# Kernel optimization log

Hardware: AMD Instinct MI355X
Metric: run time of the kernel (lower is better)

## Reference

```python
import jax, jax.numpy as jnp
import numpy as np

D_MODEL = 1024
N_HEADS = 16


def setup_inputs() -> dict:
    key = jax.random.key(0)
    ks = jax.random.split(key, 11)
    B, L, D = 2, 2048, D_MODEL
    s = 1.0 / np.sqrt(D)
    return {
        "q": jax.random.normal(ks[0], (B, L, D), jnp.float32),
        "k": jax.random.normal(ks[1], (B, L, D), jnp.float32),
        "v": jax.random.normal(ks[2], (B, L, D), jnp.float32),
        "w_q": jax.random.normal(ks[3], (D, D), jnp.float32) * s,
        "b_q": jnp.zeros((D,), jnp.float32),
        "w_k": jax.random.normal(ks[4], (D, D), jnp.float32) * s,
        "b_k": jnp.zeros((D,), jnp.float32),
        "w_v": jax.random.normal(ks[5], (D, D), jnp.float32) * s,
        "b_v": jnp.zeros((D,), jnp.float32),
        "w_o": jax.random.normal(ks[6], (D, D), jnp.float32) * s,
        "b_o": jnp.zeros((D,), jnp.float32),
    }


def reference(q, k, v, w_q, b_q, w_k, b_k, w_v, b_v, w_o, b_o):
    B, L, D = q.shape
    H = N_HEADS
    d_h = D // H
    # QKV projections (nn.Linear: x @ W^T + b)
    qh = (q @ w_q.T + b_q).reshape(B, L, H, d_h).transpose(0, 2, 1, 3)  # [B,H,L,d_h]
    kh = (k @ w_k.T + b_k).reshape(B, L, H, d_h).transpose(0, 2, 1, 3)
    vh = (v @ w_v.T + b_v).reshape(B, L, H, d_h).transpose(0, 2, 1, 3)
    # scaled dot-product attention
    scores = jnp.einsum('bhqd,bhkd->bhqk', qh, kh) / jnp.sqrt(jnp.float32(d_h))
    attn = jax.nn.softmax(scores, axis=-1)                               # [B,H,L,L]
    ctx = jnp.einsum('bhqk,bhkd->bhqd', attn, vh)                        # [B,H,L,d_h]
    ctx = ctx.transpose(0, 2, 1, 3).reshape(B, L, D)
    out = ctx @ w_o.T + b_o
    return out, attn
```

## Files before the change

### kernel.cpp

```cpp
#include <hip/hip_runtime.h>
#include <hip/hip_bf16.h>
#include <stdint.h>

#define DEV static __device__ __forceinline__

typedef float f32x4 __attribute__((ext_vector_type(4)));
typedef __bf16 bf16x8 __attribute__((ext_vector_type(8)));
typedef unsigned short u16x8 __attribute__((ext_vector_type(8)));
typedef unsigned short u16x4 __attribute__((ext_vector_type(4)));
typedef uint32_t u32x2 __attribute__((ext_vector_type(2)));
typedef uint32_t u32x4 __attribute__((ext_vector_type(4)));
typedef unsigned short u16;

#define B_ 2
#define L_ 2048
#define D_MODEL_ 1024
#define H_ 16
#define DH_ 64

#define SHIFT2 11.5415603f

DEV u16 f2bf(float f) {
  union { float f; uint32_t u; } v; v.f = f;
  uint32_t r = v.u + 0x7FFFu + ((v.u >> 16) & 1u);
  return (u16)(r >> 16);
}

DEV float exp2v(float x) {
#if __has_builtin(__builtin_amdgcn_exp2f)
  return __builtin_amdgcn_exp2f(x);
#else
  float r;
  asm("v_exp_f32 %0, %1" : "=v"(r) : "v"(x));
  return r;
#endif
}

DEV uint32_t pkbf(float a, float b) {
  __hip_bfloat162 h = __float22bfloat162_rn(float2{a, b});
  union { __hip_bfloat162 h; uint32_t u; } cv; cv.h = h;
  return cv.u;
}

DEV f32x4 mfma16(bf16x8 a, bf16x8 b, f32x4 c) {
  return __builtin_amdgcn_mfma_f32_16x16x32_bf16(a, b, c, 0, 0, 0);
}

DEV void gl_lds16(const void* g, void* l) {
  __builtin_amdgcn_global_load_lds(
      (const __attribute__((address_space(1))) unsigned int*)g,
      (__attribute__((address_space(3))) unsigned int*)l, 16, 0, 0);
}

struct CastArgs {
  const float* src[7];
  u16* dst[7];
  int n8[7];
};

__global__ __launch_bounds__(256) void cast_kernel(CastArgs a) {
  const int z = blockIdx.z;
  const float* s = a.src[z];
  u16* d = a.dst[z];
  const int n8 = a.n8[z];
  const int stride = gridDim.x * blockDim.x;
  for (int i = blockIdx.x * blockDim.x + threadIdx.x; i < n8; i += stride) {
    const float4* sp = (const float4*)s + (size_t)i * 2;
    float4 x0 = sp[0], x1 = sp[1];
    u16x8 o;
    o[0] = f2bf(x0.x); o[1] = f2bf(x0.y); o[2] = f2bf(x0.z); o[3] = f2bf(x0.w);
    o[4] = f2bf(x1.x); o[5] = f2bf(x1.y); o[6] = f2bf(x1.z); o[7] = f2bf(x1.w);
    *((u16x8*)d + i) = o;
  }
}

#define GM 4096
#define GN 1024
#define GK 1024

struct GemmArgs {
  const u16* X[3];
  const u16* W[3];
  const float* bias[3];
  void* out[3];
  float alpha[3];
  int mode[3];
};

__global__ __launch_bounds__(256) void gemm_bt(GemmArgs g) {
  const int z = blockIdx.z;
  const u16* X = g.X[z];
  const u16* W = g.W[z];
  const float* bias = g.bias[z];
  const float alpha = g.alpha[z];
  const int mode = g.mode[z];
  const int m0 = blockIdx.y * 128, n0 = blockIdx.x * 128;

  __shared__ __align__(16) char smem[32 * 1024];
  char* As = smem;
  char* Bs = smem + 16 * 1024;

  const int tid = threadIdx.x;
  const int lane = tid & 63, w = tid >> 6;
  const int l15 = lane & 15, l4 = lane >> 4;
  const int wm = (w >> 1) * 64, wn = (w & 1) * 64;

  f32x4 acc[4][4];
#pragma unroll
  for (int i = 0; i < 4; ++i)
#pragma unroll
    for (int j = 0; j < 4; ++j) acc[i][j] = f32x4{0.f, 0.f, 0.f, 0.f};

  for (int ks = 0; ks < GK; ks += 64) {
    __syncthreads();
    for (int c = w; c < 16; c += 4) {
      int r = c * 8 + (lane >> 3);
      int j = lane & 7;
      int sj = j ^ (r & 7);
      gl_lds16((const char*)(X + (size_t)(m0 + r) * GK + ks) + sj * 16, As + c * 1024);
      gl_lds16((const char*)(W + (size_t)(n0 + r) * GK + ks) + sj * 16, Bs + c * 1024);
    }
    __syncthreads();
#pragma unroll
    for (int ksub = 0; ksub < 2; ++ksub) {
      bf16x8 af[4], bfr[4];
#pragma unroll
      for (int mf = 0; mf < 4; ++mf) {
        int r = wm + mf * 16 + l15;
        int j16 = ksub * 4 + l4;
        af[mf] = *(const bf16x8*)(As + r * 128 + ((j16 ^ (r & 7)) * 16));
      }
#pragma unroll
      for (int nf = 0; nf < 4; ++nf) {
        int r = wn + nf * 16 + l15;
        int j16 = ksub * 4 + l4;
        bfr[nf] = *(const bf16x8*)(Bs + r * 128 + ((j16 ^ (r & 7)) * 16));
      }
#pragma unroll
      for (int mf = 0; mf < 4; ++mf)
#pragma unroll
        for (int nf = 0; nf < 4; ++nf) acc[mf][nf] = mfma16(af[mf], bfr[nf], acc[mf][nf]);
    }
  }

  if (mode == 2) {
    u16* base = (u16*)g.out[z];
#pragma unroll
    for (int nf = 0; nf < 4; ++nf) {
      int n = n0 + wn + nf * 16 + l15;
      float bv = bias[n];
#pragma unroll
      for (int mf = 0; mf < 4; ++mf) {
        int m = m0 + wm + mf * 16 + l4 * 4;
        u16x4 pk;
#pragma unroll
        for (int r = 0; r < 4; ++r) pk[r] = f2bf((acc[mf][nf][r] + bv) * alpha);
        size_t off = (((size_t)(m >> 11) * H_ + (n >> 6)) * DH_ + (n & 63)) * (size_t)L_ + (m & 2047);
        *(u16x4*)(base + off) = pk;
      }
    }
  } else {
#pragma unroll
    for (int nf = 0; nf < 4; ++nf) {
      int n = n0 + wn + nf * 16 + l15;
      float bv = bias[n];
#pragma unroll
      for (int mf = 0; mf < 4; ++mf) {
#pragma unroll
        for (int r = 0; r < 4; ++r) {
          int m = m0 + wm + mf * 16 + l4 * 4 + r;
          float val = (acc[mf][nf][r] + bv) * alpha;
          if (mode == 1)
            ((float*)g.out[z])[(size_t)m * GN + n] = val;
          else
            ((u16*)g.out[z])[(size_t)m * GN + n] = f2bf(val);
        }
      }
    }
  }
}

__global__ __launch_bounds__(256) void attn_kernel(const u16* Qp, const u16* Kp,
                                                   const u16* VT, float* attn,
                                                   u16* ctx) {
  const int q0 = blockIdx.x * 64;
  const int h = blockIdx.y, b = blockIdx.z;
  const int tid = threadIdx.x, lane = tid & 63, w = tid >> 6;
  const int l15 = lane & 15, l4 = lane >> 4;
  const int lr = lane >> 3, lj = lane & 7;

  __shared__ __align__(16) char smem[32 * 1024];
  char* Pw = smem + w * 4096;

  const u16* Qbase = Qp + ((size_t)(b * L_ + q0 + w * 16) * D_MODEL_ + h * DH_);
  const u16* Kbase = Kp + ((size_t)(b * L_) * D_MODEL_ + h * DH_);
  const u16* Vb = VT + ((size_t)((b * H_ + h) * DH_) * L_);
  float* attnb = attn + ((size_t)(b * H_ + h)) * L_ * L_;

  auto stK = [&](int t) {
    const int c0 = t * 64, bsel = (t & 1) << 13;
    for (int c = w; c < 8; c += 4) {
      int r = c * 8 + lr, sj = lj ^ (r & 7);
      gl_lds16((const char*)(Kbase + (size_t)(c0 + r) * D_MODEL_) + sj * 16,
               smem + 16384 + bsel + c * 1024);
    }
  };

  bf16x8 qa[2];
#pragma unroll
  for (int ksub = 0; ksub < 2; ++ksub)
    qa[ksub] = *(const bf16x8*)(Qbase + (size_t)l15 * D_MODEL_ + (ksub * 4 + l4) * 8);

  stK(0);
  __syncthreads();

  float ssum = 0.f;
  for (int t = 0; t < 32; ++t) {
    if (t < 31) stK(t + 1);
    const char* Ks = smem + 16384 + ((t & 1) << 13);
    f32x4 s[4];
#pragma unroll
    for (int nf = 0; nf < 4; ++nf) s[nf] = f32x4{0.f, 0.f, 0.f, 0.f};
    __builtin_amdgcn_s_setprio(1);
#pragma unroll
    for (int ksub = 0; ksub < 2; ++ksub) {
      int j16 = ksub * 4 + l4;
      bf16x8 kb[4];
#pragma unroll
      for (int nf = 0; nf < 4; ++nf) {
        int r = nf * 16 + l15;
        kb[nf] = *(const bf16x8*)(Ks + r * 128 + ((j16 ^ (r & 7)) * 16));
      }
#pragma unroll
      for (int nf = 0; nf < 4; ++nf) s[nf] = mfma16(kb[nf], qa[ksub], s[nf]);
    }
    __builtin_amdgcn_s_setprio(0);
#pragma unroll
    for (int nf = 0; nf < 4; ++nf)
#pragma unroll
      for (int r = 0; r < 4; ++r) ssum += exp2v(s[nf][r] - SHIFT2);
    __syncthreads();
  }

  stK(0);

  ssum += __shfl_xor(ssum, 16);
  ssum += __shfl_xor(ssum, 32);
  const float c2 = SHIFT2 + __log2f(ssum);

  f32x4 cacc[4];
#pragma unroll
  for (int i = 0; i < 4; ++i) cacc[i] = f32x4{0.f, 0.f, 0.f, 0.f};
  __syncthreads();

  const int swz = l15 & 7;
  float* awave = attnb + (size_t)(q0 + w * 16) * L_;

  for (int t = 0; t < 32; ++t) {
    const int c0 = t * 64;
    if (t < 31) stK(t + 1);
    bf16x8 va[2][4];
#pragma unroll
    for (int ksub = 0; ksub < 2; ++ksub)
#pragma unroll
      for (int df = 0; df < 4; ++df)
        va[ksub][df] = *(const bf16x8*)(Vb + (size_t)(df * 16 + l15) * L_ + c0 +
                                        (ksub * 4 + l4) * 8);
    __builtin_amdgcn_sched_barrier(0);

    const char* Ks = smem + 16384 + ((t & 1) << 13);
    f32x4 s[4];
#pragma unroll
    for (int nf = 0; nf < 4; ++nf) s[nf] = f32x4{0.f, 0.f, 0.f, 0.f};
    __builtin_amdgcn_s_setprio(1);
#pragma unroll
    for (int ksub = 0; ksub < 2; ++ksub) {
      int j16 = ksub * 4 + l4;
      bf16x8 kb[4];
#pragma unroll
      for (int nf = 0; nf < 4; ++nf) {
        int r = nf * 16 + l15;
        kb[nf] = *(const bf16x8*)(Ks + r * 128 + ((j16 ^ (r & 7)) * 16));
      }
#pragma unroll
      for (int nf = 0; nf < 4; ++nf) s[nf] = mfma16(kb[nf], qa[ksub], s[nf]);
    }
    __builtin_amdgcn_s_setprio(0);

#pragma unroll
    for (int nf = 0; nf < 4; ++nf) {
      f32x4 p4;
#pragma unroll
      for (int r = 0; r < 4; ++r) p4[r] = exp2v(s[nf][r] - c2);
      *(f32x4*)(Pw + l15 * 256 + (((nf * 4 + l4) ^ swz) * 16)) = p4;
    }
#pragma unroll
    for (int j = 0; j < 4; ++j) {
      int row = 4 * j + (lane >> 4);
      f32x4 v = *(const f32x4*)(Pw + row * 256 + (((lane & 15) ^ (row & 7)) * 16));
      __builtin_nontemporal_store(
          v, (f32x4*)(awave + (size_t)row * L_ + c0 + (lane & 15) * 4));
    }
    __builtin_amdgcn_s_setprio(1);
#pragma unroll
    for (int ksub = 0; ksub < 2; ++ksub) {
      int cbase = (ksub * 4 + l4) * 2;
      f32x4 plo = *(const f32x4*)(Pw + l15 * 256 + ((cbase ^ swz) * 16));
      f32x4 phi = *(const f32x4*)(Pw + l15 * 256 + (((cbase + 1) ^ swz) * 16));
      union { u32x4 u; bf16x8 h; } pa;
      pa.u[0] = pkbf(plo[0], plo[1]);
      pa.u[1] = pkbf(plo[2], plo[3]);
      pa.u[2] = pkbf(phi[0], phi[1]);
      pa.u[3] = pkbf(phi[2], phi[3]);
#pragma unroll
      for (int df = 0; df < 4; ++df)
        cacc[df] = mfma16(pa.h, va[ksub][df], cacc[df]);
    }
    __builtin_amdgcn_s_setprio(0);
    if (t < 31) {
      asm volatile("s_waitcnt vmcnt(12)" ::: "memory");
      __builtin_amdgcn_s_barrier();
      __builtin_amdgcn_sched_barrier(0);
    }
  }

#pragma unroll
  for (int df = 0; df < 4; ++df) {
#pragma unroll
    for (int r = 0; r < 4; ++r) {
      int row = q0 + w * 16 + l4 * 4 + r;
      int col = h * DH_ + df * 16 + l15;
      ctx[(size_t)(b * L_ + row) * D_MODEL_ + col] = f2bf(cacc[df][r]);
    }
  }
}

extern "C" void kernel_launch(void* const* d_in, const int* in_sizes, int n_in,
                              void* d_out, int out_size, void* d_ws, size_t ws_size,
                              hipStream_t stream) {
  const float* q = (const float*)d_in[0];
  const float* k = (const float*)d_in[1];
  const float* v = (const float*)d_in[2];
  const float* w_q = (const float*)d_in[3];
  const float* b_q = (const float*)d_in[4];
  const float* w_k = (const float*)d_in[5];
  const float* b_k = (const float*)d_in[6];
  const float* w_v = (const float*)d_in[7];
  const float* b_v = (const float*)d_in[8];
  const float* w_o = (const float*)d_in[9];
  const float* b_o = (const float*)d_in[10];

  float* out = (float*)d_out;
  float* attn = (float*)d_out + (size_t)B_ * L_ * D_MODEL_;

  const size_t MB = 1u << 20;
  char* ws = (char*)d_ws;
  u16* qb = (u16*)(ws + 0 * MB);
  u16* kb = (u16*)(ws + 8 * MB);
  u16* vb = (u16*)(ws + 16 * MB);
  u16* wqb = (u16*)(ws + 24 * MB);
  u16* wkb = (u16*)(ws + 26 * MB);
  u16* wvb = (u16*)(ws + 28 * MB);
  u16* wob = (u16*)(ws + 30 * MB);
  u16* Qp = (u16*)(ws + 32 * MB);
  u16* Kp = (u16*)(ws + 40 * MB);
  u16* VT = (u16*)(ws + 48 * MB);
  u16* ctx = kb;

  CastArgs ca;
  ca.src[0] = q;   ca.dst[0] = qb;  ca.n8[0] = (B_ * L_ * D_MODEL_) / 8;
  ca.src[1] = k;   ca.dst[1] = kb;  ca.n8[1] = (B_ * L_ * D_MODEL_) / 8;
  ca.src[2] = v;   ca.dst[2] = vb;  ca.n8[2] = (B_ * L_ * D_MODEL_) / 8;
  ca.src[3] = w_q; ca.dst[3] = wqb; ca.n8[3] = (D_MODEL_ * D_MODEL_) / 8;
  ca.src[4] = w_k; ca.dst[4] = wkb; ca.n8[4] = (D_MODEL_ * D_MODEL_) / 8;
  ca.src[5] = w_v; ca.dst[5] = wvb; ca.n8[5] = (D_MODEL_ * D_MODEL_) / 8;
  ca.src[6] = w_o; ca.dst[6] = wob; ca.n8[6] = (D_MODEL_ * D_MODEL_) / 8;
  cast_kernel<<<dim3(1024, 1, 7), 256, 0, stream>>>(ca);

  GemmArgs ga;
  ga.X[0] = qb;  ga.W[0] = wqb; ga.bias[0] = b_q; ga.out[0] = Qp; ga.alpha[0] = 0.125f * 1.44269504f; ga.mode[0] = 0;
  ga.X[1] = kb;  ga.W[1] = wkb; ga.bias[1] = b_k; ga.out[1] = Kp; ga.alpha[1] = 1.f;    ga.mode[1] = 0;
  ga.X[2] = vb;  ga.W[2] = wvb; ga.bias[2] = b_v; ga.out[2] = VT; ga.alpha[2] = 1.f;    ga.mode[2] = 2;
  gemm_bt<<<dim3(8, 32, 3), 256, 0, stream>>>(ga);

  attn_kernel<<<dim3(32, 16, 2), 256, 0, stream>>>(Qp, Kp, VT, attn, ctx);

  GemmArgs go;
  go.X[0] = ctx; go.W[0] = wob; go.bias[0] = b_o; go.out[0] = out; go.alpha[0] = 1.f; go.mode[0] = 1;
  go.X[1] = ctx; go.W[1] = wob; go.bias[1] = b_o; go.out[1] = out; go.alpha[1] = 1.f; go.mode[1] = 1;
  go.X[2] = ctx; go.W[2] = wob; go.bias[2] = b_o; go.out[2] = out; go.alpha[2] = 1.f; go.mode[2] = 1;
  gemm_bt<<<dim3(8, 32, 1), 256, 0, stream>>>(go);
}
```

Measured before the change: 275.0 us.

## Split softmax denominator pass into separate key-chunked kernel with atomic sums

Moves the first pass of the attention kernel, which computes per-row sums of exp of the scores, into a new kernel. That kernel splits the key dimension into four chunks, giving four times as many blocks, and combines the partial sums with atomicAdd into a workspace buffer. The cast kernel gains an extra slice that zeroes this buffer. The aim is more parallelism and a shorter serial loop in the attention kernel. The cost is an extra launch, atomics, and recomputing QK^T in a separate pass as before.

```diff
diff --git a/kernel.cpp b/kernel.cpp
--- a/kernel.cpp
+++ b/kernel.cpp
@@ -53,17 +53,22 @@
 }
 
 struct CastArgs {
-  const float* src[7];
-  u16* dst[7];
-  int n8[7];
+  const float* src[8];
+  u16* dst[8];
+  int n8[8];
 };
 
 __global__ __launch_bounds__(256) void cast_kernel(CastArgs a) {
   const int z = blockIdx.z;
-  const float* s = a.src[z];
   u16* d = a.dst[z];
   const int n8 = a.n8[z];
   const int stride = gridDim.x * blockDim.x;
+  if (z == 7) {
+    for (int i = blockIdx.x * blockDim.x + threadIdx.x; i < n8; i += stride)
+      *((u16x8*)d + i) = u16x8{0, 0, 0, 0, 0, 0, 0, 0};
+    return;
+  }
+  const float* s = a.src[z];
   for (int i = blockIdx.x * blockDim.x + threadIdx.x; i < n8; i += stride) {
     const float4* sp = (const float4*)s + (size_t)i * 2;
     float4 x0 = sp[0], x1 = sp[1];
@@ -180,9 +185,73 @@
   }
 }
 
+__global__ __launch_bounds__(256) void sumexp_kernel(const u16* Qp, const u16* Kp,
+                                                     float* sums) {
+  const int q0 = blockIdx.x * 64;
+  const int kc0 = blockIdx.y * 512;
+  const int bh = blockIdx.z;
+  const int b = bh >> 4, h = bh & 15;
+  const int tid = threadIdx.x, lane = tid & 63, w = tid >> 6;
+  const int l15 = lane & 15, l4 = lane >> 4;
+  const int lr = lane >> 3, lj = lane & 7;
+
+  __shared__ __align__(16) char smem[16 * 1024];
+
+  const u16* Qbase = Qp + ((size_t)(b * L_ + q0 + w * 16) * D_MODEL_ + h * DH_);
+  const u16* Kbase = Kp + ((size_t)(b * L_ + kc0) * D_MODEL_ + h * DH_);
+
+  auto stK = [&](int t) {
+    const int c0 = t * 64, bsel = (t & 1) << 13;
+    for (int c = w; c < 8; c += 4) {
+      int r = c * 8 + lr, sj = lj ^ (r & 7);
+      gl_lds16((const char*)(Kbase + (size_t)(c0 + r) * D_MODEL_) + sj * 16,
+               smem + bsel + c * 1024);
+    }
+  };
+
+  bf16x8 qa[2];
+#pragma unroll
+  for (int ksub = 0; ksub < 2; ++ksub)
+    qa[ksub] = *(const bf16x8*)(Qbase + (size_t)l15 * D_MODEL_ + (ksub * 4 + l4) * 8);
+
+  stK(0);
+  __syncthreads();
+
+  float ssum = 0.f;
+  for (int t = 0; t < 8; ++t) {
+    if (t < 7) stK(t + 1);
+    const char* Ks = smem + ((t & 1) << 13);
+    f32x4 s[4];
+#pragma unroll
+    for (int nf = 0; nf < 4; ++nf) s[nf] = f32x4{0.f, 0.f, 0.f, 0.f};
+#pragma unroll
+    for (int ksub = 0; ksub < 2; ++ksub) {
+      int j16 = ksub * 4 + l4;
+      bf16x8 kb[4];
+#pragma unroll
+      for (int nf = 0; nf < 4; ++nf) {
+        int r = nf * 16 + l15;
+        kb[nf] = *(const bf16x8*)(Ks + r * 128 + ((j16 ^ (r & 7)) * 16));
+      }
+#pragma unroll
+      for (int nf = 0; nf < 4; ++nf) s[nf] = mfma16(kb[nf], qa[ksub], s[nf]);
+    }
+#pragma unroll
+    for (int nf = 0; nf < 4; ++nf)
+#pragma unroll
+      for (int r = 0; r < 4; ++r) ssum += exp2v(s[nf][r] - SHIFT2);
+    __syncthreads();
+  }
+
+  ssum += __shfl_xor(ssum, 16);
+  ssum += __shfl_xor(ssum, 32);
+  if (lane < 16)
+    atomicAdd(&sums[((size_t)bh << 11) + q0 + w * 16 + lane], ssum);
+}
+
 __global__ __launch_bounds__(256) void attn_kernel(const u16* Qp, const u16* Kp,
-                                                   const u16* VT, float* attn,
-                                                   u16* ctx) {
+                                                   const u16* VT, const float* sums,
+                                                   float* attn, u16* ctx) {
   const int q0 = blockIdx.x * 64;
   const int h = blockIdx.y, b = blockIdx.z;
   const int tid = threadIdx.x, lane = tid & 63, w = tid >> 6;
@@ -211,50 +280,18 @@
   for (int ksub = 0; ksub < 2; ++ksub)
     qa[ksub] = *(const bf16x8*)(Qbase + (size_t)l15 * D_MODEL_ + (ksub * 4 + l4) * 8);
 
+  const float c2 =
+      SHIFT2 + __log2f(sums[(((size_t)(b * H_ + h)) << 11) + q0 + w * 16 + l15]);
+
   stK(0);
-  __syncthreads();
-
-  float ssum = 0.f;
-  for (int t = 0; t < 32; ++t) {
-    if (t < 31) stK(t + 1);
-    const char* Ks = smem + 16384 + ((t & 1) << 13);
-    f32x4 s[4];
-#pragma unroll
-    for (int nf = 0; nf < 4; ++nf) s[nf] = f32x4{0.f, 0.f, 0.f, 0.f};
-    __builtin_amdgcn_s_setprio(1);
-#pragma unroll
-    for (int ksub = 0; ksub < 2; ++ksub) {
-      int j16 = ksub * 4 + l4;
-      bf16x8 kb[4];
-#pragma unroll
-      for (int nf = 0; nf < 4; ++nf) {
-        int r = nf * 16 + l15;
-        kb[nf] = *(const bf16x8*)(Ks + r * 128 + ((j16 ^ (r & 7)) * 16));
-      }
-#pragma unroll
-      for (int nf = 0; nf < 4; ++nf) s[nf] = mfma16(kb[nf], qa[ksub], s[nf]);
-    }
-    __builtin_amdgcn_s_setprio(0);
-#pragma unroll
-    for (int nf = 0; nf < 4; ++nf)
-#pragma unroll
-      for (int r = 0; r < 4; ++r) ssum += exp2v(s[nf][r] - SHIFT2);
-    __syncthreads();
-  }
-
-  stK(0);
-
-  ssum += __shfl_xor(ssum, 16);
-  ssum += __shfl_xor(ssum, 32);
-  const float c2 = SHIFT2 + __log2f(ssum);
 
   f32x4 cacc[4];
 #pragma unroll
   for (int i = 0; i < 4; ++i) cacc[i] = f32x4{0.f, 0.f, 0.f, 0.f};
-  __syncthreads();
 
   const int swz = l15 & 7;
   float* awave = attnb + (size_t)(q0 + w * 16) * L_;
+  __syncthreads();
 
   for (int t = 0; t < 32; ++t) {
     const int c0 = t * 64;
@@ -365,6 +402,7 @@
   u16* Qp = (u16*)(ws + 32 * MB);
   u16* Kp = (u16*)(ws + 40 * MB);
   u16* VT = (u16*)(ws + 48 * MB);
+  float* sums = (float*)(ws + 56 * MB);
   u16* ctx = kb;
 
   CastArgs ca;
@@ -375,7 +413,8 @@
   ca.src[4] = w_k; ca.dst[4] = wkb; ca.n8[4] = (D_MODEL_ * D_MODEL_) / 8;
   ca.src[5] = w_v; ca.dst[5] = wvb; ca.n8[5] = (D_MODEL_ * D_MODEL_) / 8;
   ca.src[6] = w_o; ca.dst[6] = wob; ca.n8[6] = (D_MODEL_ * D_MODEL_) / 8;
-  cast_kernel<<<dim3(1024, 1, 7), 256, 0, stream>>>(ca);
+  ca.src[7] = nullptr; ca.dst[7] = (u16*)sums; ca.n8[7] = (B_ * H_ * L_ * 4) / 16;
+  cast_kernel<<<dim3(1024, 1, 8), 256, 0, stream>>>(ca);
 
   GemmArgs ga;
   ga.X[0] = qb;  ga.W[0] = wqb; ga.bias[0] = b_q; ga.out[0] = Qp; ga.alpha[0] = 0.125f * 1.44269504f; ga.mode[0] = 0;
@@ -383,7 +422,9 @@
   ga.X[2] = vb;  ga.W[2] = wvb; ga.bias[2] = b_v; ga.out[2] = VT; ga.alpha[2] = 1.f;    ga.mode[2] = 2;
   gemm_bt<<<dim3(8, 32, 3), 256, 0, stream>>>(ga);
 
-  attn_kernel<<<dim3(32, 16, 2), 256, 0, stream>>>(Qp, Kp, VT, attn, ctx);
+  sumexp_kernel<<<dim3(32, 4, 32), 256, 0, stream>>>(Qp, Kp, sums);
+
+  attn_kernel<<<dim3(32, 16, 2), 256, 0, stream>>>(Qp, Kp, VT, sums, attn, ctx);
 
   GemmArgs go;
   go.X[0] = ctx; go.W[0] = wob; go.bias[0] = b_o; go.out[0] = out; go.alpha[0] = 1.f; go.mode[0] = 1;
```

Result: no change. 276.2 us (+0.4%).
